# Kernel tuning notes

Hardware: AMD Instinct MI355X
Metric: run time of the kernel (lower is better)

The kernel has to match this reference:

```python
import jax, jax.numpy as jnp
import numpy as np

N_NODES = 100000
N_EDGES = 600000
IN_DIM, HID, OUT = 6, 128, 1
EPS = 1e-5


def _glorot(key, shape):
    fan_in, fan_out = shape[1], shape[0]
    lim = jnp.sqrt(6.0 / (fan_in + fan_out))
    return jax.random.uniform(key, shape, jnp.float32, -lim, lim)


def setup_inputs() -> dict:
    key = jax.random.key(0)
    ks = jax.random.split(key, 16)
    x = jax.random.normal(ks[0], (N_NODES, IN_DIM), jnp.float32)
    edge_index = jax.random.randint(ks[1], (2, N_EDGES), 0, N_NODES, jnp.int64)
    return {
        "x": x,
        "edge_index": edge_index,
        # SAGEConv layer 0: 6 -> 128 (lin_l acts on aggregated neighbors, lin_r on root)
        "w_l0": _glorot(ks[2], (HID, IN_DIM)), "b_l0": jnp.zeros((HID,), jnp.float32),
        "w_r0": _glorot(ks[3], (HID, IN_DIM)),
        "bn_g0": jnp.ones((HID,), jnp.float32), "bn_b0": jnp.zeros((HID,), jnp.float32),
        # SAGEConv layer 1: 128 -> 128
        "w_l1": _glorot(ks[4], (HID, HID)), "b_l1": jnp.zeros((HID,), jnp.float32),
        "w_r1": _glorot(ks[5], (HID, HID)),
        "bn_g1": jnp.ones((HID,), jnp.float32), "bn_b1": jnp.zeros((HID,), jnp.float32),
        # SAGEConv layer 2: 128 -> 1
        "w_l2": _glorot(ks[6], (OUT, HID)), "b_l2": jnp.zeros((OUT,), jnp.float32),
        "w_r2": _glorot(ks[7], (OUT, HID)),
    }


def _sage_conv(x, src, dst, inv_deg, w_l, b_l, w_r):
    # mean aggregation of source-node features into destination nodes
    agg = jax.ops.segment_sum(x[src], dst, num_segments=N_NODES)  # [N, d]
    mean_nb = agg * inv_deg[:, None]
    return mean_nb @ w_l.T + b_l + x @ w_r.T


def _batch_norm(x, gamma, beta):
    mu = jnp.mean(x, axis=0)
    var = jnp.mean(jnp.square(x - mu), axis=0)  # biased, as torch BN training
    return (x - mu) * jax.lax.rsqrt(var + EPS) * gamma + beta


def reference(x, edge_index, w_l0, b_l0, w_r0, bn_g0, bn_b0,
              w_l1, b_l1, w_r1, bn_g1, bn_b1, w_l2, b_l2, w_r2):
    src, dst = edge_index[0], edge_index[1]
    deg = jax.ops.segment_sum(jnp.ones_like(dst, dtype=x.dtype), dst,
                              num_segments=N_NODES)
    inv_deg = 1.0 / jnp.maximum(deg, 1.0)

    h = _sage_conv(x, src, dst, inv_deg, w_l0, b_l0, w_r0)
    h = jax.nn.relu(_batch_norm(h, bn_g0, bn_b0))  # dropout = identity (eval)

    h = _sage_conv(h, src, dst, inv_deg, w_l1, b_l1, w_r1)
    h = jax.nn.relu(_batch_norm(h, bn_g1, bn_b1))

    h = _sage_conv(h, src, dst, inv_deg, w_l2, b_l2, w_r2)
    return jax.nn.sigmoid(h).squeeze(-1)  # [N]
```

## Files before the change

### kernel.cpp

```cpp
#include <hip/hip_runtime.h>
#include <math.h>

#define HID 128
#define INDIM 6

typedef float4 f4;
typedef __attribute__((ext_vector_type(8))) short short8;
typedef __attribute__((ext_vector_type(4))) float f32x4;

static __device__ inline unsigned short f2bf(float f) {
    union { float f; unsigned int u; } v; v.f = f;
    unsigned int r = v.u + 0x7fffu + ((v.u >> 16) & 1u);
    return (unsigned short)(r >> 16);
}
static __device__ inline float bf2f_lo(unsigned int u) {
    union { unsigned int u; float f; } v; v.u = u << 16; return v.f;
}
static __device__ inline float bf2f_hi(unsigned int u) {
    union { unsigned int u; float f; } v; v.u = u & 0xffff0000u; return v.f;
}

__global__ void k_zero2(int* a, int na, int* b, int nb) {
    int i = blockIdx.x * blockDim.x + threadIdx.x;
    if (i < na) a[i] = 0;
    if (i < nb) b[i] = 0;
}

__global__ void k_deg(const int* dst, int* deg, int* rank, int E) {
    int e = blockIdx.x * blockDim.x + threadIdx.x;
    if (e < E) rank[e] = atomicAdd(&deg[dst[e]], 1);
}

__global__ void k_scan_partial(const int* __restrict__ deg, int* __restrict__ partial, int N) {
    __shared__ int lds[256];
    int t = threadIdx.x;
    int base = blockIdx.x * 1024 + t * 4;
    int s = 0;
    if (base + 4 <= N) {
        int4 v = *(const int4*)&deg[base];
        s = v.x + v.y + v.z + v.w;
    } else {
        for (int i = 0; i < 4; i++) if (base + i < N) s += deg[base + i];
    }
    lds[t] = s;
    __syncthreads();
    for (int off = 128; off > 0; off >>= 1) {
        if (t < off) lds[t] += lds[t + off];
        __syncthreads();
    }
    if (t == 0) partial[blockIdx.x] = lds[0];
}

__global__ void k_scan_tops(int* partial, int nb) {
    __shared__ int lds[1024];
    int t = threadIdx.x;
    lds[t] = (t < nb) ? partial[t] : 0;
    __syncthreads();
    for (int off = 1; off < 1024; off <<= 1) {
        int v = (t >= off) ? lds[t - off] : 0;
        __syncthreads();
        lds[t] += v;
        __syncthreads();
    }
    if (t < nb) partial[t] = (t == 0) ? 0 : lds[t - 1];
}

__global__ void k_scan_write(const int* __restrict__ deg, const int* __restrict__ partial,
                             int* __restrict__ rowptr, int N, int E) {
    __shared__ int lds[256];
    int t = threadIdx.x;
    int base = blockIdx.x * 1024 + t * 4;
    int v0 = 0, v1 = 0, v2 = 0, v3 = 0;
    if (base + 4 <= N) {
        int4 v = *(const int4*)&deg[base];
        v0 = v.x; v1 = v.y; v2 = v.z; v3 = v.w;
    } else {
        if (base + 0 < N) v0 = deg[base + 0];
        if (base + 1 < N) v1 = deg[base + 1];
        if (base + 2 < N) v2 = deg[base + 2];
        if (base + 3 < N) v3 = deg[base + 3];
    }
    lds[t] = v0 + v1 + v2 + v3;
    __syncthreads();
    for (int off = 1; off < 256; off <<= 1) {
        int v = (t >= off) ? lds[t - off] : 0;
        __syncthreads();
        lds[t] += v;
        __syncthreads();
    }
    int run = partial[blockIdx.x] + ((t == 0) ? 0 : lds[t - 1]);
    if (base + 0 < N) rowptr[base + 0] = run; run += v0;
    if (base + 1 < N) rowptr[base + 1] = run; run += v1;
    if (base + 2 < N) rowptr[base + 2] = run; run += v2;
    if (base + 3 < N) rowptr[base + 3] = run; run += v3;
    if (blockIdx.x == 0 && t == 0) rowptr[N] = E;
}

__global__ void k_fill(const int* ei, const int* rank, const int* rowptr, int* csr, int E) {
    int e = blockIdx.x * blockDim.x + threadIdx.x;
    if (e < E) {
        int d = ei[E + e];
        csr[rowptr[d] + rank[e]] = ei[e];
    }
}

__global__ void k_invdeg(const int* deg, float* invd, int N) {
    int i = blockIdx.x * blockDim.x + threadIdx.x;
    if (i < N) invd[i] = 1.0f / (float)max(deg[i], 1);
}

__global__ void k_prepw(const float* __restrict__ wl, const float* __restrict__ wr,
                        unsigned short* __restrict__ wcat) {
    int i = blockIdx.x * 256 + threadIdx.x;
    int o = i >> 8, k = i & 255;
    float v = (k < 128) ? wl[o * 128 + k] : wr[o * 128 + k - 128];
    wcat[i] = f2bf(v);
}

__global__ __launch_bounds__(256) void k_l0stats(
        const float* __restrict__ x, const int* __restrict__ rowptr,
        const int* __restrict__ csr, const float* __restrict__ invd,
        const float* __restrict__ wl, const float* __restrict__ bl,
        const float* __restrict__ wr, float* __restrict__ mean6,
        float* __restrict__ sum8, float* __restrict__ sq8, int N) {
    __shared__ float wlds[1600];
    __shared__ float blds[136];
    __shared__ float mx[32][8];
    __shared__ float xr[32][8];
    __shared__ float ps[4][128];
    __shared__ float pq[4][128];
    int t = threadIdx.x;
    for (int idx = t; idx < 1536; idx += 256) {
        int half = idx >= 768 ? 1 : 0;
        int lin = idx - half * 768;
        int o = lin / 6, i = lin - o * 6;
        float v = half ? wr[lin] : wl[lin];
        wlds[half * 800 + o * 6 + i + (o >> 4) * 2] = v;
    }
    if (t < 128) blds[t + (t >> 4)] = bl[t];
    int nl = t >> 3, f = t & 7;
    int n = blockIdx.x * 32 + nl;
    bool valid = n < N;
    if (f < 6) {
        float mean = 0.f, xv = 0.f;
        if (valid) {
            int s = rowptr[n], e = rowptr[n + 1];
            float acc = 0.f;
            int i = s;
            for (; i + 4 <= e; i += 4) {
                int i0 = csr[i], i1 = csr[i + 1], i2 = csr[i + 2], i3 = csr[i + 3];
                float a0 = x[i0 * 6 + f], a1 = x[i1 * 6 + f];
                float a2 = x[i2 * 6 + f], a3 = x[i3 * 6 + f];
                acc += (a0 + a1) + (a2 + a3);
            }
            for (; i < e; i++) acc += x[csr[i] * 6 + f];
            mean = acc * invd[n];
            xv = x[n * 6 + f];
            mean6[n * 6 + f] = mean;
        }
        mx[nl][f] = mean;
        xr[nl][f] = xv;
    }
    __syncthreads();
    float m0 = mx[nl][0], m1 = mx[nl][1], m2 = mx[nl][2];
    float m3 = mx[nl][3], m4 = mx[nl][4], m5 = mx[nl][5];
    float r0 = xr[nl][0], r1 = xr[nl][1], r2 = xr[nl][2];
    float r3 = xr[nl][3], r4 = xr[nl][4], r5 = xr[nl][5];
    const float* wA = wlds;
    const float* wB = wlds + 800;
    int wv = t >> 6, lane = t & 63;
#pragma unroll
    for (int k = 0; k < 16; k++) {
        int o = f * 16 + k;
        int wb = 98 * f + 6 * k;
        float h = blds[o + f];
        h += m0 * wA[wb] + m1 * wA[wb + 1] + m2 * wA[wb + 2]
           + m3 * wA[wb + 3] + m4 * wA[wb + 4] + m5 * wA[wb + 5];
        h += r0 * wB[wb] + r1 * wB[wb + 1] + r2 * wB[wb + 2]
           + r3 * wB[wb + 3] + r4 * wB[wb + 4] + r5 * wB[wb + 5];
        float s = valid ? h : 0.f;
        float q = s * s;
        s += __shfl_xor(s, 8, 64);  q += __shfl_xor(q, 8, 64);
        s += __shfl_xor(s, 16, 64); q += __shfl_xor(q, 16, 64);
        s += __shfl_xor(s, 32, 64); q += __shfl_xor(q, 32, 64);
        if (lane < 8) { ps[wv][lane * 16 + k] = s; pq[wv][lane * 16 + k] = q; }
    }
    __syncthreads();
    if (t < 128) {
        float S = ps[0][t] + ps[1][t] + ps[2][t] + ps[3][t];
        float Q = pq[0][t] + pq[1][t] + pq[2][t] + pq[3][t];
        int slot = (blockIdx.x & 7) * 128 + t;
        atomicAdd(&sum8[slot], S);
        atomicAdd(&sq8[slot], Q);
    }
}

__global__ __launch_bounds__(256) void k_l0apply(
        const float* __restrict__ x, const float* __restrict__ mean6,
        const float* __restrict__ wl, const float* __restrict__ bl,
        const float* __restrict__ wr, const float* __restrict__ scale,
        const float* __restrict__ shift, unsigned short* __restrict__ out, int N) {
    __shared__ float wlds[1600];
    __shared__ float blds[136];
    __shared__ float sclds[136];
    __shared__ float shlds[136];
    __shared__ float mx[32][8];
    __shared__ float xr[32][8];
    int t = threadIdx.x;
    for (int idx = t; idx < 1536; idx += 256) {
        int half = idx >= 768 ? 1 : 0;
        int lin = idx - half * 768;
        int o = lin / 6, i = lin - o * 6;
        float v = half ? wr[lin] : wl[lin];
        wlds[half * 800 + o * 6 + i + (o >> 4) * 2] = v;
    }
    if (t < 128) {
        blds[t + (t >> 4)]  = bl[t];
        sclds[t + (t >> 4)] = scale[t];
        shlds[t + (t >> 4)] = shift[t];
    }
    int nl = t >> 3, f = t & 7;
    int n = blockIdx.x * 32 + nl;
    bool valid = n < N;
    if (f < 6) {
        mx[nl][f] = valid ? mean6[n * 6 + f] : 0.f;
        xr[nl][f] = valid ? x[n * 6 + f] : 0.f;
    }
    __syncthreads();
    if (!valid) return;
    float m0 = mx[nl][0], m1 = mx[nl][1], m2 = mx[nl][2];
    float m3 = mx[nl][3], m4 = mx[nl][4], m5 = mx[nl][5];
    float r0 = xr[nl][0], r1 = xr[nl][1], r2 = xr[nl][2];
    float r3 = xr[nl][3], r4 = xr[nl][4], r5 = xr[nl][5];
    const float* wA = wlds;
    const float* wB = wlds + 800;
    unsigned short pk[16];
#pragma unroll
    for (int k4 = 0; k4 < 4; k4++) {
#pragma unroll
        for (int j = 0; j < 4; j++) {
            int k = k4 * 4 + j;
            int o = f * 16 + k;
            int wb = 98 * f + 6 * k;
            float h = blds[o + f];
            h += m0 * wA[wb] + m1 * wA[wb + 1] + m2 * wA[wb + 2]
               + m3 * wA[wb + 3] + m4 * wA[wb + 4] + m5 * wA[wb + 5];
            h += r0 * wB[wb] + r1 * wB[wb + 1] + r2 * wB[wb + 2]
               + r3 * wB[wb + 3] + r4 * wB[wb + 4] + r5 * wB[wb + 5];
            pk[k] = f2bf(fmaxf(0.f, fmaf(h, sclds[o + f], shlds[o + f])));
        }
    }
    unsigned short* dst = out + (size_t)n * HID + f * 16;
    *(uint4*)(dst)     = *(const uint4*)&pk[0];
    *(uint4*)(dst + 8) = *(const uint4*)&pk[8];
}

__global__ void k_bnfin8(const float* sum8, const float* sq8, const float* g, const float* b,
                         float* scale, float* shift, float invN) {
    int t = threadIdx.x;
    float s = 0.f, q = 0.f;
    for (int c = 0; c < 8; c++) { s += sum8[c * 128 + t]; q += sq8[c * 128 + t]; }
    float mu  = s * invN;
    float var = q * invN - mu * mu;
    float sc  = g[t] * rsqrtf(var + 1e-5f);
    scale[t] = sc;
    shift[t] = b[t] - mu * sc;
}

__global__ void k_agg_bf(const unsigned short* __restrict__ hb, const int* __restrict__ rowptr,
                         const int* __restrict__ csr, const float* __restrict__ invd,
                         unsigned short* __restrict__ out, int N) {
    int t = threadIdx.x;
    int w = t >> 6, lid = t & 63;
    int half = lid >> 5, l32 = lid & 31;
    int n = blockIdx.x * 8 + w * 2 + half;
    if (n >= N) return;
    int s = rowptr[n], e = rowptr[n + 1];
    const uint2* hb64 = (const uint2*)hb;
    float ax0 = 0.f, ay0 = 0.f, ax1 = 0.f, ay1 = 0.f;
    int i = s;
    for (; i + 4 <= e; i += 4) {
        int i0 = csr[i], i1 = csr[i + 1], i2 = csr[i + 2], i3 = csr[i + 3];
        uint2 u0 = hb64[(size_t)i0 * 32 + l32];
        uint2 u1 = hb64[(size_t)i1 * 32 + l32];
        uint2 u2 = hb64[(size_t)i2 * 32 + l32];
        uint2 u3 = hb64[(size_t)i3 * 32 + l32];
        ax0 += (bf2f_lo(u0.x) + bf2f_lo(u1.x)) + (bf2f_lo(u2.x) + bf2f_lo(u3.x));
        ay0 += (bf2f_hi(u0.x) + bf2f_hi(u1.x)) + (bf2f_hi(u2.x) + bf2f_hi(u3.x));
        ax1 += (bf2f_lo(u0.y) + bf2f_lo(u1.y)) + (bf2f_lo(u2.y) + bf2f_lo(u3.y));
        ay1 += (bf2f_hi(u0.y) + bf2f_hi(u1.y)) + (bf2f_hi(u2.y) + bf2f_hi(u3.y));
    }
    for (; i < e; i++) {
        uint2 u = hb64[(size_t)csr[i] * 32 + l32];
        ax0 += bf2f_lo(u.x); ay0 += bf2f_hi(u.x);
        ax1 += bf2f_lo(u.y); ay1 += bf2f_hi(u.y);
    }
    float id = invd[n];
    uint2 r;
    r.x = (unsigned int)f2bf(ax0 * id) | ((unsigned int)f2bf(ay0 * id) << 16);
    r.y = (unsigned int)f2bf(ax1 * id) | ((unsigned int)f2bf(ay1 * id) << 16);
    ((uint2*)out)[(size_t)n * 32 + l32] = r;
}

__global__ __launch_bounds__(256) void k_gemm(
        const unsigned short* __restrict__ Bm, const unsigned short* __restrict__ Ar,
        const unsigned short* __restrict__ wcat, const float* __restrict__ bias,
        float* __restrict__ sum8, float* __restrict__ sq8,
        float* __restrict__ C, int N) {
    __shared__ __align__(16) unsigned short As[128][40];
    __shared__ __align__(16) unsigned short Ws[128][40];
    __shared__ float lds_s[2][128];
    __shared__ float lds_q[2][128];
    int t = threadIdx.x;
    int wave = t >> 6, lane = t & 63;
    int wr = wave >> 1, wc = wave & 1;
    int row0 = blockIdx.x * 128;
    int r = t >> 1, half = t & 1;

    f32x4 acc[4][4];
#pragma unroll
    for (int m = 0; m < 4; m++)
#pragma unroll
        for (int n = 0; n < 4; n++) acc[m][n] = (f32x4)(0.f);

    for (int chunk = 0; chunk < 8; chunk++) {
        int kb = chunk * 32;
        int srow = row0 + r;
        int c0 = (chunk & 3) * 32 + half * 16;
        const unsigned short* src = (chunk < 4) ? Bm : Ar;
        if (srow < N) {
            const unsigned short* p = src + (size_t)srow * HID + c0;
            *(uint4*)&As[r][half * 16]     = *(const uint4*)(p);
            *(uint4*)&As[r][half * 16 + 8] = *(const uint4*)(p + 8);
        } else {
            uint4 z = make_uint4(0, 0, 0, 0);
            *(uint4*)&As[r][half * 16]     = z;
            *(uint4*)&As[r][half * 16 + 8] = z;
        }
        const unsigned short* wp = wcat + r * 256 + kb + half * 16;
        *(uint4*)&Ws[r][half * 16]     = *(const uint4*)(wp + 0);
        *(uint4*)&Ws[r][half * 16 + 8] = *(const uint4*)(wp + 8);
        __syncthreads();

        int lrow = lane & 15, koff = (lane >> 4) * 8;
        short8 af[4], bfr[4];
#pragma unroll
        for (int m = 0; m < 4; m++)
            af[m] = *(const short8*)&As[wr * 64 + m * 16 + lrow][koff];
#pragma unroll
        for (int n = 0; n < 4; n++)
            bfr[n] = *(const short8*)&Ws[wc * 64 + n * 16 + lrow][koff];
#pragma unroll
        for (int m = 0; m < 4; m++)
#pragma unroll
            for (int n = 0; n < 4; n++)
                acc[m][n] = __builtin_amdgcn_mfma_f32_16x16x32_bf16(af[m], bfr[n], acc[m][n], 0, 0, 0);
        __syncthreads();
    }

    int cl = lane & 15, rq = (lane >> 4) * 4;
    float cs[4], cq[4];
#pragma unroll
    for (int n = 0; n < 4; n++) {
        int col = wc * 64 + n * 16 + cl;
        float bn = bias[col];
        float s = 0.f, q = 0.f;
#pragma unroll
        for (int m = 0; m < 4; m++) {
#pragma unroll
            for (int reg = 0; reg < 4; reg++) {
                int row = row0 + wr * 64 + m * 16 + rq + reg;
                float v = acc[m][n][reg] + bn;
                if (row < N) {
                    C[(size_t)row * HID + col] = v;
                    s += v;
                    q += v * v;
                }
            }
        }
        cs[n] = s; cq[n] = q;
    }
#pragma unroll
    for (int n = 0; n < 4; n++) {
        float s = cs[n], q = cq[n];
        s += __shfl_xor(s, 16, 64); q += __shfl_xor(q, 16, 64);
        s += __shfl_xor(s, 32, 64); q += __shfl_xor(q, 32, 64);
        if (lane < 16) {
            int col = wc * 64 + n * 16 + cl;
            lds_s[wr][col] = s;
            lds_q[wr][col] = q;
        }
    }
    __syncthreads();
    if (t < 128) {
        float S = lds_s[0][t] + lds_s[1][t];
        float Q = lds_q[0][t] + lds_q[1][t];
        int slot = (blockIdx.x & 7) * 128 + t;
        atomicAdd(&sum8[slot], S);
        atomicAdd(&sq8[slot], Q);
    }
}

__global__ void k_dots(const float* __restrict__ h, const float* __restrict__ scale,
                       const float* __restrict__ shift, const float* __restrict__ wl2,
                       const float* __restrict__ wr2, float* __restrict__ s_arr,
                       float* __restrict__ r_arr, int N) {
    int w = threadIdx.x >> 6, lid = threadIdx.x & 63;
    int n = blockIdx.x * 4 + w;
    if (n >= N) return;
    float2 v  = *(const float2*)&h[(size_t)n * HID + lid * 2];
    float2 sc = *(const float2*)&scale[lid * 2];
    float2 sh = *(const float2*)&shift[lid * 2];
    float y0 = fmaxf(0.f, fmaf(v.x, sc.x, sh.x));
    float y1 = fmaxf(0.f, fmaf(v.y, sc.y, sh.y));
    float2 wl = *(const float2*)&wl2[lid * 2];
    float2 wrv = *(const float2*)&wr2[lid * 2];
    float ps = y0 * wl.x + y1 * wl.y;
    float pr = y0 * wrv.x + y1 * wrv.y;
#pragma unroll
    for (int off = 32; off > 0; off >>= 1) {
        ps += __shfl_down(ps, off, 64);
        pr += __shfl_down(pr, off, 64);
    }
    if (lid == 0) { s_arr[n] = ps; r_arr[n] = pr; }
}

__global__ void k_final2(const float* __restrict__ s_arr, const float* __restrict__ r_arr,
                         const int* __restrict__ rowptr, const int* __restrict__ csr,
                         const float* __restrict__ invd, const float* __restrict__ bl2,
                         float* __restrict__ out, int N) {
    int n = blockIdx.x * blockDim.x + threadIdx.x;
    if (n >= N) return;
    int s = rowptr[n], e = rowptr[n + 1];
    float a = 0.f;
    int i = s;
    for (; i + 4 <= e; i += 4) {
        float a0 = s_arr[csr[i]],     a1 = s_arr[csr[i + 1]];
        float a2 = s_arr[csr[i + 2]], a3 = s_arr[csr[i + 3]];
        a += (a0 + a1) + (a2 + a3);
    }
    for (; i < e; i++) a += s_arr[csr[i]];
    float p = a * invd[n] + r_arr[n] + bl2[0];
    out[n] = 1.f / (1.f + expf(-p));
}

extern "C" void kernel_launch(void* const* d_in, const int* in_sizes, int n_in,
                              void* d_out, int out_size, void* d_ws, size_t ws_size,
                              hipStream_t stream) {
    const float* x   = (const float*)d_in[0];
    const int*   ei  = (const int*)d_in[1];
    const float* wl0 = (const float*)d_in[2];
    const float* bl0 = (const float*)d_in[3];
    const float* wr0 = (const float*)d_in[4];
    const float* g0  = (const float*)d_in[5];
    const float* be0 = (const float*)d_in[6];
    const float* wl1 = (const float*)d_in[7];
    const float* bl1 = (const float*)d_in[8];
    const float* wr1 = (const float*)d_in[9];
    const float* g1  = (const float*)d_in[10];
    const float* be1 = (const float*)d_in[11];
    const float* wl2 = (const float*)d_in[12];
    const float* bl2 = (const float*)d_in[13];
    const float* wr2 = (const float*)d_in[14];
    float* outp = (float*)d_out;

    int N = in_sizes[0] / INDIM;
    int E = in_sizes[1] / 2;

    char* ws = (char*)d_ws;
    size_t off = 0;
    auto alloc = [&](size_t bytes) { size_t o = off; off = (off + bytes + 255) & ~(size_t)255; return o; };
    int*   degi   = (int*)(ws + alloc((size_t)N * 4));
    int*   rank   = (int*)(ws + alloc((size_t)E * 4));
    int*   rowptr = (int*)(ws + alloc((size_t)(N + 1) * 4));
    int*   csr    = (int*)(ws + alloc((size_t)E * 4));
    float* invd   = (float*)(ws + alloc((size_t)N * 4));
    int*   partial= (int*)(ws + alloc(1024 * 4));
    float* bnbuf  = (float*)(ws + alloc(5120 * 4));
    unsigned short* wcat = (unsigned short*)(ws + alloc(128 * 256 * 2));
    float* sarr   = (float*)(ws + alloc((size_t)N * 4));
    float* rarr   = (float*)(ws + alloc((size_t)N * 4));
    float* mean6  = (float*)(ws + alloc((size_t)N * 6 * 4));
    float* sum0_8 = bnbuf;
    float* sq0_8  = bnbuf + 1024;
    float* sum1_8 = bnbuf + 2048;
    float* sq1_8  = bnbuf + 3072;
    float* sc0 = bnbuf + 4096, *sh0 = bnbuf + 4224;
    float* sc1 = bnbuf + 4352, *sh1 = bnbuf + 4480;
    float* bufB = (float*)(ws + alloc((size_t)N * HID * 4));
    unsigned short* bufC = (unsigned short*)(ws + alloc((size_t)N * HID * 2));
    unsigned short* bufD = (unsigned short*)(ws + alloc((size_t)N * HID * 2));

    float invN = 1.0f / (float)N;
    int gE = (E + 255) / 256;
    int gN = (N + 255) / 256;
    int gW = (N + 3) / 4;
    int gA = (N + 7) / 8;
    int gL = (N + 31) / 32;
    int gS = (N + 127) / 128;
    int nbScan = (N + 1023) / 1024;

    k_zero2<<<gN, 256, 0, stream>>>(degi, N, (int*)bnbuf, 4096);

    k_prepw<<<128, 256, 0, stream>>>(wl1, wr1, wcat);

    k_deg<<<gE, 256, 0, stream>>>(ei + E, degi, rank, E);
    k_scan_partial<<<nbScan, 256, 0, stream>>>(degi, partial, N);
    k_scan_tops<<<1, 1024, 0, stream>>>(partial, nbScan);
    k_scan_write<<<nbScan, 256, 0, stream>>>(degi, partial, rowptr, N, E);
    k_fill<<<gE, 256, 0, stream>>>(ei, rank, rowptr, csr, E);
    k_invdeg<<<gN, 256, 0, stream>>>(degi, invd, N);

    k_l0stats<<<gL, 256, 0, stream>>>(x, rowptr, csr, invd, wl0, bl0, wr0, mean6,
                                      sum0_8, sq0_8, N);
    k_bnfin8<<<1, 128, 0, stream>>>(sum0_8, sq0_8, g0, be0, sc0, sh0, invN);

    k_l0apply<<<gL, 256, 0, stream>>>(x, mean6, wl0, bl0, wr0, sc0, sh0, bufC, N);

    k_agg_bf<<<gA, 256, 0, stream>>>(bufC, rowptr, csr, invd, bufD, N);
    k_gemm<<<gS, 256, 0, stream>>>(bufD, bufC, wcat, bl1, sum1_8, sq1_8, bufB, N);
    k_bnfin8<<<1, 128, 0, stream>>>(sum1_8, sq1_8, g1, be1, sc1, sh1, invN);

    k_dots<<<gW, 256, 0, stream>>>(bufB, sc1, sh1, wl2, wr2, sarr, rarr, N);
    k_final2<<<gN, 256, 0, stream>>>(sarr, rarr, rowptr, csr, invd, bl2, outp, N);
}
```

Baseline: 210.1 us.

## Store layer-1 GEMM output as bf16 and read weights directly from global

The layer-1 GEMM now writes its 128-wide output as bf16 instead of fp32, and k_dots reads the bf16 values. This halves the write and read traffic of the largest intermediate buffer. The GEMM K-loop is also restructured: 64-wide chunks cut the loop from eight to four iterations, halving the syncs, and the weight B-fragments are loaded straight from global/L2 instead of being staged in LDS. BN statistics are still computed from the fp32 values, so the normalized activations that feed the dot products carry bf16 rounding.

```diff
diff --git a/kernel.cpp b/kernel.cpp
--- a/kernel.cpp
+++ b/kernel.cpp
@@ -306,9 +306,8 @@
         const unsigned short* __restrict__ Bm, const unsigned short* __restrict__ Ar,
         const unsigned short* __restrict__ wcat, const float* __restrict__ bias,
         float* __restrict__ sum8, float* __restrict__ sq8,
-        float* __restrict__ C, int N) {
-    __shared__ __align__(16) unsigned short As[128][40];
-    __shared__ __align__(16) unsigned short Ws[128][40];
+        unsigned short* __restrict__ C, int N) {
+    __shared__ __align__(16) unsigned short As[128][72];
     __shared__ float lds_s[2][128];
     __shared__ float lds_q[2][128];
     int t = threadIdx.x;
@@ -316,6 +315,7 @@
     int wr = wave >> 1, wc = wave & 1;
     int row0 = blockIdx.x * 128;
     int r = t >> 1, half = t & 1;
+    int lrow = lane & 15, koff = (lane >> 4) * 8;
 
     f32x4 acc[4][4];
 #pragma unroll
@@ -323,38 +323,40 @@
 #pragma unroll
         for (int n = 0; n < 4; n++) acc[m][n] = (f32x4)(0.f);
 
-    for (int chunk = 0; chunk < 8; chunk++) {
-        int kb = chunk * 32;
+    for (int chunk = 0; chunk < 4; chunk++) {
+        int kb = chunk * 64;
         int srow = row0 + r;
-        int c0 = (chunk & 3) * 32 + half * 16;
-        const unsigned short* src = (chunk < 4) ? Bm : Ar;
+        int c0 = (kb & 127) + half * 32;
+        const unsigned short* src = (kb < 128) ? Bm : Ar;
+        uint4 v0, v1, v2, v3;
         if (srow < N) {
             const unsigned short* p = src + (size_t)srow * HID + c0;
-            *(uint4*)&As[r][half * 16]     = *(const uint4*)(p);
-            *(uint4*)&As[r][half * 16 + 8] = *(const uint4*)(p + 8);
+            v0 = *(const uint4*)(p);      v1 = *(const uint4*)(p + 8);
+            v2 = *(const uint4*)(p + 16); v3 = *(const uint4*)(p + 24);
         } else {
-            uint4 z = make_uint4(0, 0, 0, 0);
-            *(uint4*)&As[r][half * 16]     = z;
-            *(uint4*)&As[r][half * 16 + 8] = z;
+            v0 = v1 = v2 = v3 = make_uint4(0, 0, 0, 0);
         }
-        const unsigned short* wp = wcat + r * 256 + kb + half * 16;
-        *(uint4*)&Ws[r][half * 16]     = *(const uint4*)(wp + 0);
-        *(uint4*)&Ws[r][half * 16 + 8] = *(const uint4*)(wp + 8);
-        __syncthreads();
-
-        int lrow = lane & 15, koff = (lane >> 4) * 8;
-        short8 af[4], bfr[4];
-#pragma unroll
-        for (int m = 0; m < 4; m++)
-            af[m] = *(const short8*)&As[wr * 64 + m * 16 + lrow][koff];
-#pragma unroll
-        for (int n = 0; n < 4; n++)
-            bfr[n] = *(const short8*)&Ws[wc * 64 + n * 16 + lrow][koff];
-#pragma unroll
-        for (int m = 0; m < 4; m++)
+        *(uint4*)&As[r][half * 32]      = v0;
+        *(uint4*)&As[r][half * 32 + 8]  = v1;
+        *(uint4*)&As[r][half * 32 + 16] = v2;
+        *(uint4*)&As[r][half * 32 + 24] = v3;
+        __syncthreads();
+
+#pragma unroll
+        for (int ks = 0; ks < 64; ks += 32) {
+            short8 af[4], bfr[4];
+#pragma unroll
+            for (int m = 0; m < 4; m++)
+                af[m] = *(const short8*)&As[wr * 64 + m * 16 + lrow][ks + koff];
 #pragma unroll
             for (int n = 0; n < 4; n++)
-                acc[m][n] = __builtin_amdgcn_mfma_f32_16x16x32_bf16(af[m], bfr[n], acc[m][n], 0, 0, 0);
+                bfr[n] = *(const short8*)&wcat[(size_t)(wc * 64 + n * 16 + lrow) * 256 + kb + ks + koff];
+#pragma unroll
+            for (int m = 0; m < 4; m++)
+#pragma unroll
+                for (int n = 0; n < 4; n++)
+                    acc[m][n] = __builtin_amdgcn_mfma_f32_16x16x32_bf16(af[m], bfr[n], acc[m][n], 0, 0, 0);
+        }
         __syncthreads();
     }
 
@@ -372,7 +374,7 @@
                 int row = row0 + wr * 64 + m * 16 + rq + reg;
                 float v = acc[m][n][reg] + bn;
                 if (row < N) {
-                    C[(size_t)row * HID + col] = v;
+                    C[(size_t)row * HID + col] = f2bf(v);
                     s += v;
                     q += v * v;
                 }
@@ -401,18 +403,19 @@
     }
 }
 
-__global__ void k_dots(const float* __restrict__ h, const float* __restrict__ scale,
+__global__ void k_dots(const unsigned short* __restrict__ h, const float* __restrict__ scale,
                        const float* __restrict__ shift, const float* __restrict__ wl2,
                        const float* __restrict__ wr2, float* __restrict__ s_arr,
                        float* __restrict__ r_arr, int N) {
     int w = threadIdx.x >> 6, lid = threadIdx.x & 63;
     int n = blockIdx.x * 4 + w;
     if (n >= N) return;
-    float2 v  = *(const float2*)&h[(size_t)n * HID + lid * 2];
+    unsigned int u = ((const unsigned int*)h)[(size_t)n * 64 + lid];
+    float hx = bf2f_lo(u), hy = bf2f_hi(u);
     float2 sc = *(const float2*)&scale[lid * 2];
     float2 sh = *(const float2*)&shift[lid * 2];
-    float y0 = fmaxf(0.f, fmaf(v.x, sc.x, sh.x));
-    float y1 = fmaxf(0.f, fmaf(v.y, sc.y, sh.y));
+    float y0 = fmaxf(0.f, fmaf(hx, sc.x, sh.x));
+    float y1 = fmaxf(0.f, fmaf(hy, sc.y, sh.y));
     float2 wl = *(const float2*)&wl2[lid * 2];
     float2 wrv = *(const float2*)&wr2[lid * 2];
     float ps = y0 * wl.x + y1 * wl.y;
@@ -487,7 +490,7 @@
     float* sq1_8  = bnbuf + 3072;
     float* sc0 = bnbuf + 4096, *sh0 = bnbuf + 4224;
     float* sc1 = bnbuf + 4352, *sh1 = bnbuf + 4480;
-    float* bufB = (float*)(ws + alloc((size_t)N * HID * 4));
+    unsigned short* bufB = (unsigned short*)(ws + alloc((size_t)N * HID * 2));
     unsigned short* bufC = (unsigned short*)(ws + alloc((size_t)N * HID * 2));
     unsigned short* bufD = (unsigned short*)(ws + alloc((size_t)N * HID * 2));
 
```

Result: slower. 214.8 us (+2.2%).
